# Optimization experiments

Hardware: AMD Instinct MI355X
Metric: run time of the kernel (lower is better)

Reference implementation:

```python
import jax, jax.numpy as jnp
import numpy as np

EMBED_DIM = 1024
NUM_HEADS = 16
HEAD_DIM = EMBED_DIM // NUM_HEADS


def setup_inputs() -> dict:
    key = jax.random.key(0)
    ks = jax.random.split(key, 11)
    B, S, D = 2, 2048, EMBED_DIM
    s = 1.0 / np.sqrt(D)
    inp = {
        "query": jax.random.normal(ks[0], (B, S, D), jnp.float32),
        "key": jax.random.normal(ks[1], (B, S, D), jnp.float32),
        "value": jax.random.normal(ks[2], (B, S, D), jnp.float32),
        # torch Linear weights: [out, in]
        "Wq": jax.random.normal(ks[3], (D, D), jnp.float32) * s,
        "bq": jnp.zeros((D,), jnp.float32),
        "Wk": jax.random.normal(ks[4], (D, D), jnp.float32) * s,
        "bk": jnp.zeros((D,), jnp.float32),
        "Wv": jax.random.normal(ks[5], (D, D), jnp.float32) * s,
        "bv": jnp.zeros((D,), jnp.float32),
        "Wo": jax.random.normal(ks[6], (D, D), jnp.float32) * s,
        "bo": jnp.zeros((D,), jnp.float32),
    }
    return inp


def reference(query, key, value, Wq, bq, Wk, bk, Wv, bv, Wo, bo):
    B, Q, D = query.shape
    K = key.shape[1]
    H, Hd = NUM_HEADS, HEAD_DIM
    # NOTE: source divides by scaling = head_dim**-0.5, i.e. multiplies by sqrt(head_dim)
    scaling = float(Hd) ** (-0.5)

    q = (query @ Wq.T + bq).reshape(B, Q, H, Hd).transpose(0, 2, 1, 3)  # [B,H,Q,Hd]
    k = (key @ Wk.T + bk).reshape(B, K, H, Hd).transpose(0, 2, 1, 3)    # [B,H,K,Hd]
    v = (value @ Wv.T + bv).reshape(B, K, H, Hd).transpose(0, 2, 1, 3)  # [B,H,K,Hd]

    scores = jnp.einsum("bhqd,bhkd->bhqk", q, k) / scaling
    attn = jax.nn.softmax(scores, axis=-1)  # dropout=0 (eval)
    out = jnp.einsum("bhqk,bhkd->bhqd", attn, v)
    out = out.transpose(0, 2, 1, 3).reshape(B, Q, D)
    return out @ Wo.T + bo
```

## Files before the change

### kernel.cpp

```cpp
#include <hip/hip_runtime.h>
#include <type_traits>
#include <utility>

#define B_ 2
#define S_ 2048
#define D_ 1024
#define H_ 16
#define HD_ 64
#define KDIM 1024

typedef __attribute__((ext_vector_type(8))) short    s16x8;
typedef __attribute__((ext_vector_type(8))) _Float16 h16x8;
typedef __attribute__((ext_vector_type(4))) float    f32x4;
typedef __attribute__((ext_vector_type(4))) int      i32x4;
typedef __attribute__((ext_vector_type(2))) int      i32x2;

template <typename T, typename = void> struct mfma_takes : std::false_type {};
template <typename T>
struct mfma_takes<T, std::void_t<decltype(__builtin_amdgcn_mfma_f32_16x16x32_f16(
    std::declval<T>(), std::declval<T>(), std::declval<f32x4>(), 0, 0, 0))>>
    : std::true_type {};
using frag8 = std::conditional_t<mfma_takes<h16x8>::value, h16x8, s16x8>;

__device__ __forceinline__ f32x4 mfma_f16(frag8 a, frag8 b, f32x4 c) {
  return __builtin_amdgcn_mfma_f32_16x16x32_f16(a, b, c, 0, 0, 0);
}

__device__ __forceinline__ short f2h(float f) {
  _Float16 h = (_Float16)f;
  short s; __builtin_memcpy(&s, &h, 2);
  return s;
}
__device__ __forceinline__ int pk2h(float a, float b) {
  auto p = __builtin_amdgcn_cvt_pkrtz(a, b);
  int r; __builtin_memcpy(&r, &p, 4); return r;
}
__device__ __forceinline__ frag8 ld_frag(const short* p) {
  return __builtin_bit_cast(frag8, *(const i32x4*)p);
}
__device__ __forceinline__ float fast_exp2(float x) {
  return __builtin_amdgcn_exp2f(x);
}

typedef __attribute__((address_space(1))) const void gvoid;
typedef __attribute__((address_space(3))) void lvoid;
__device__ __forceinline__ void async_copy16(const void* g, void* l) {
  __builtin_amdgcn_global_load_lds((gvoid*)g, (lvoid*)l, 16, 0, 0);
}

#define RAW_BARRIER() asm volatile("s_barrier" ::: "memory")
#define WAITCNT_VM(n) asm volatile("s_waitcnt vmcnt(" #n ")" ::: "memory")

__global__ __launch_bounds__(256)
void conv_all(const float* __restrict__ q, const float* __restrict__ k,
              const float* __restrict__ v, const float* __restrict__ Wq,
              const float* __restrict__ Wk, const float* __restrict__ Wv,
              const float* __restrict__ Wo,
              short* __restrict__ qh, short* __restrict__ kh,
              short* __restrict__ vh, short* __restrict__ wq,
              short* __restrict__ wk, short* __restrict__ wv,
              short* __restrict__ wo) {
  const int blk = blockIdx.x;
  const float* src; short* dst; int base;
  if (blk < 2048)      { src = q;  dst = qh; base = blk; }
  else if (blk < 4096) { src = k;  dst = kh; base = blk - 2048; }
  else if (blk < 6144) { src = v;  dst = vh; base = blk - 4096; }
  else if (blk < 6656) { src = Wq; dst = wq; base = blk - 6144; }
  else if (blk < 7168) { src = Wk; dst = wk; base = blk - 6656; }
  else if (blk < 7680) { src = Wv; dst = wv; base = blk - 7168; }
  else                 { src = Wo; dst = wo; base = blk - 7680; }
  const int i = base * 2048 + threadIdx.x * 8;
  float4 a0 = *(const float4*)(src + i);
  float4 a1 = *(const float4*)(src + i + 4);
  short h[8] = { f2h(a0.x), f2h(a0.y), f2h(a0.z), f2h(a0.w),
                 f2h(a1.x), f2h(a1.y), f2h(a1.z), f2h(a1.w) };
  i32x4 ph; __builtin_memcpy(&ph, h, 16);
  *(i32x4*)(dst + i) = ph;
}

__global__ __launch_bounds__(256, 3)
void gemm_qkv(const short* __restrict__ qh, const short* __restrict__ kh,
              const short* __restrict__ vh, const short* __restrict__ wq,
              const short* __restrict__ wk, const short* __restrict__ wv,
              const float* __restrict__ bq, const float* __restrict__ bk,
              const float* __restrict__ bv, short* __restrict__ Qf,
              short* __restrict__ Kf, short* __restrict__ Vt, float QS) {
  __shared__ short As[3 * 4096];
  __shared__ short Bs[3 * 4096];

  const int blk = blockIdx.x;
  const int xcd = blk & 7, i = blk >> 3;
  const int p = (i >> 3) * 8 + xcd;
  const int bn = i & 7;
  const int z = p >> 5, bm = p & 31;
  const short* Ap = z == 0 ? qh : z == 1 ? kh : vh;
  const short* Wp = z == 0 ? wq : z == 1 ? wk : wv;
  const float* bias = z == 0 ? bq : z == 1 ? bk : bv;
  short* Out = z == 0 ? Qf : z == 1 ? Kf : Vt;
  const float scale = z == 0 ? QS : 1.0f;
  const int omode = z == 2 ? 2 : 1;

  const int t = threadIdx.x, wave = t >> 6, lane = t & 63;
  const int laneN = lane & 15, quad = lane >> 4;
  const int wm = wave & 1, wn = wave >> 1;

  f32x4 acc[4][4];
#pragma unroll
  for (int i2 = 0; i2 < 4; ++i2)
#pragma unroll
    for (int j = 0; j < 4; ++j)
#pragma unroll
      for (int r = 0; r < 4; ++r) acc[i2][j][r] = 0.f;

  auto stage = [&](int buf, int kk) {
#pragma unroll
    for (int j = 0; j < 2; ++j) {
      const int chunk = j * 256 + t;
      const int row = chunk >> 2;
      const int gg = (chunk & 3) ^ ((row >> 1) & 3);
      async_copy16(Ap + (size_t)(bm * 128 + row) * KDIM + kk + gg * 8,
                   As + buf * 4096 + chunk * 8);
      async_copy16(Wp + (size_t)(bn * 128 + row) * KDIM + kk + gg * 8,
                   Bs + buf * 4096 + chunk * 8);
    }
  };

  stage(0, 0);
  stage(1, 32);
  int buf = 0;
  for (int kk = 0; kk < KDIM; kk += 32) {
    if (kk + 64 < KDIM) {
      int nb = buf + 2; if (nb >= 3) nb -= 3;
      stage(nb, kk + 64);
      WAITCNT_VM(8);
    } else if (kk + 32 < KDIM) {
      WAITCNT_VM(4);
    } else {
      WAITCNT_VM(0);
    }
    RAW_BARRIER();

    frag8 aF[4], bF[4];
#pragma unroll
    for (int mi = 0; mi < 4; ++mi) {
      const int row = wm * 64 + mi * 16 + laneN;
      aF[mi] = ld_frag(As + buf * 4096 + row * 32 +
                       ((quad ^ ((row >> 1) & 3)) * 8));
    }
#pragma unroll
    for (int ni = 0; ni < 4; ++ni) {
      const int row = wn * 64 + ni * 16 + laneN;
      bF[ni] = ld_frag(Bs + buf * 4096 + row * 32 +
                       ((quad ^ ((row >> 1) & 3)) * 8));
    }
#pragma unroll
    for (int mi = 0; mi < 4; ++mi)
#pragma unroll
      for (int ni = 0; ni < 4; ++ni)
        acc[mi][ni] = mfma_f16(aF[mi], bF[ni], acc[mi][ni]);
    RAW_BARRIER();
    buf = buf + 1 == 3 ? 0 : buf + 1;
  }

  short* scr = As + wave * 1152;
  const int h = bn * 2 + wn;
  if (omode == 2) {
    const int bidx = bm >> 4;
    const int sbase = (bm * 128 + wm * 64) & 2047;
#pragma unroll
    for (int ni = 0; ni < 4; ++ni) {
      const float bb = bias[bn * 128 + wn * 64 + ni * 16 + laneN];
#pragma unroll
      for (int mi = 0; mi < 4; ++mi) {
        short pk[4];
#pragma unroll
        for (int r = 0; r < 4; ++r) pk[r] = f2h(acc[mi][ni][r] + bb);
        i32x2 w; __builtin_memcpy(&w, pk, 8);
        *(i32x2*)(scr + laneN * 72 + mi * 16 + quad * 4) = w;
      }
#pragma unroll
      for (int j = 0; j < 2; ++j) {
        const int ff = lane * 2 + j, hdr = ff >> 3, ch = ff & 7;
        i32x4 v = *(const i32x4*)(scr + hdr * 72 + ch * 8);
        *(i32x4*)(Vt + (((size_t)(bidx * H_ + h)) * HD_ + ni * 16 + hdr) * S_ +
                  sbase + ch * 8) = v;
      }
    }
  } else {
#pragma unroll
    for (int mi = 0; mi < 4; ++mi) {
#pragma unroll
      for (int ni = 0; ni < 4; ++ni) {
        const float bb = bias[bn * 128 + wn * 64 + ni * 16 + laneN];
#pragma unroll
        for (int r = 0; r < 4; ++r)
          scr[(quad * 4 + r) * 72 + ni * 16 + laneN] =
              f2h((acc[mi][ni][r] + bb) * scale);
      }
#pragma unroll
      for (int j = 0; j < 2; ++j) {
        const int ff = lane * 2 + j, row = ff >> 3, ch = ff & 7;
        const int rowg = bm * 128 + wm * 64 + mi * 16 + row;
        const int bidx = rowg >> 11, s = rowg & 2047;
        i32x4 v = *(const i32x4*)(scr + row * 72 + ch * 8);
        *(i32x4*)(Out + (((size_t)(bidx * H_ + h)) * S_ + s) * HD_ + ch * 8) = v;
      }
    }
  }
}

__global__ __launch_bounds__(256, 3)
void gemm_out(const short* __restrict__ Ap, const short* __restrict__ Wp,
              const float* __restrict__ bias, float* __restrict__ Out) {
  __shared__ short As[3 * 4096];
  __shared__ short Bs[3 * 2048];
  const int blk = blockIdx.x;
  const int xcd = blk & 7, i = blk >> 3;
  const int bm = (i >> 4) * 8 + xcd;
  const int bn = i & 15;

  const int t = threadIdx.x, wave = t >> 6, lane = t & 63;
  const int laneN = lane & 15, quad = lane >> 4;
  const int wm = wave & 1, wn = wave >> 1;

  f32x4 acc[4][2];
#pragma unroll
  for (int i2 = 0; i2 < 4; ++i2)
#pragma unroll
    for (int j = 0; j < 2; ++j)
#pragma unroll
      for (int r = 0; r < 4; ++r) acc[i2][j][r] = 0.f;

  auto stage = [&](int buf, int kk) {
#pragma unroll
    for (int j = 0; j < 2; ++j) {
      const int chunk = j * 256 + t;
      const int row = chunk >> 2;
      const int gg = (chunk & 3) ^ ((row >> 1) & 3);
      async_copy16(Ap + (size_t)(bm * 128 + row) * KDIM + kk + gg * 8,
                   As + buf * 4096 + chunk * 8);
    }
    {
      const int chunk = t;
      const int row = chunk >> 2;
      const int gg = (chunk & 3) ^ ((row >> 1) & 3);
      async_copy16(Wp + (size_t)(bn * 64 + row) * KDIM + kk + gg * 8,
                   Bs + buf * 2048 + chunk * 8);
    }
  };

  stage(0, 0);
  stage(1, 32);
  int buf = 0;
  for (int kk = 0; kk < KDIM; kk += 32) {
    if (kk + 64 < KDIM) {
      int nb = buf + 2; if (nb >= 3) nb -= 3;
      stage(nb, kk + 64);
      WAITCNT_VM(6);
    } else if (kk + 32 < KDIM) {
      WAITCNT_VM(3);
    } else {
      WAITCNT_VM(0);
    }
    RAW_BARRIER();

    frag8 aF[4], bF[2];
#pragma unroll
    for (int mi = 0; mi < 4; ++mi) {
      const int row = wm * 64 + mi * 16 + laneN;
      aF[mi] = ld_frag(As + buf * 4096 + row * 32 +
                       ((quad ^ ((row >> 1) & 3)) * 8));
    }
#pragma unroll
    for (int ni = 0; ni < 2; ++ni) {
      const int row = wn * 32 + ni * 16 + laneN;
      bF[ni] = ld_frag(Bs + buf * 2048 + row * 32 +
                       ((quad ^ ((row >> 1) & 3)) * 8));
    }
#pragma unroll
    for (int mi = 0; mi < 4; ++mi)
#pragma unroll
      for (int ni = 0; ni < 2; ++ni)
        acc[mi][ni] = mfma_f16(aF[mi], bF[ni], acc[mi][ni]);
    RAW_BARRIER();
    buf = buf + 1 == 3 ? 0 : buf + 1;
  }

  float* scr = (float*)As + wave * 576;
#pragma unroll
  for (int mi = 0; mi < 4; ++mi) {
#pragma unroll
    for (int ni = 0; ni < 2; ++ni) {
      const float bb = bias[bn * 64 + wn * 32 + ni * 16 + laneN];
#pragma unroll
      for (int r = 0; r < 4; ++r)
        scr[(quad * 4 + r) * 36 + ni * 16 + laneN] = acc[mi][ni][r] + bb;
    }
#pragma unroll
    for (int j = 0; j < 2; ++j) {
      const int ff = lane * 2 + j, row = ff >> 3, ch = ff & 7;
      const int rowg = bm * 128 + wm * 64 + mi * 16 + row;
      f32x4 v = *(const f32x4*)(scr + row * 36 + ch * 4);
      *(f32x4*)(Out + (size_t)rowg * 1024 + bn * 64 + wn * 32 + ch * 4) = v;
    }
  }
}

__global__ __launch_bounds__(512, 4)
void attn(const short* __restrict__ Qf, const short* __restrict__ Kf,
          const short* __restrict__ Vt_, short* __restrict__ Ow) {
  __shared__ short Ks[4 * 4096];
  __shared__ short Vts[4 * 4096];
  __shared__ short Ps[8][16 * 64];

  const int blk = blockIdx.x;
  const int xcd = blk & 7, local = blk >> 3;
  const int pair = xcd * 4 + (local >> 4);
  const int h = pair & 15, b = pair >> 4, qt = local & 15;
  const size_t head = ((size_t)b * H_ + h) * (size_t)S_ * HD_;

  const int t = threadIdx.x;
  const int wave = t >> 6, lane = t & 63;
  const int laneN = lane & 15, quad = lane >> 4;

  frag8 qf[2];
  {
    const size_t row = (size_t)qt * 128 + wave * 16 + laneN;
#pragma unroll
    for (int half = 0; half < 2; ++half)
      qf[half] = ld_frag(Qf + head + row * HD_ + half * 32 + quad * 8);
  }

  f32x4 o[4];
  float m_r = -1e30f, l_r = 0.f;
#pragma unroll
  for (int i = 0; i < 4; ++i)
#pragma unroll
    for (int j = 0; j < 4; ++j) o[i][j] = 0.f;

  const int srow = t >> 3, sg = (t & 7) ^ (srow & 7);
  const short* kp = Kf + head + (size_t)srow * HD_ + sg * 8;
  const short* vp = Vt_ + head + (size_t)srow * S_ + sg * 8;
  const int d = t * 8;

  int off[4][2];
#pragma unroll
  for (int nt = 0; nt < 4; ++nt) {
    const int row = nt * 16 + laneN;
    off[nt][0] = row * 64 + ((quad ^ (row & 7)) * 8);
    off[nt][1] = row * 64 + (((quad + 4) ^ (row & 7)) * 8);
  }

  short* const pwr = &Ps[wave][0] + laneN * 64;
  short* pw[4];
#pragma unroll
  for (int nt = 0; nt < 4; ++nt) {
    const int g = nt * 2 + (quad >> 1);
    pw[nt] = pwr + ((g + laneN) & 7) * 8 + (quad & 1) * 4;
  }
  const short* prd0 = pwr + ((quad + laneN) & 7) * 8;
  const short* prd1 = pwr + (((quad + 4) + laneN) & 7) * 8;

  async_copy16(kp, Ks + d);  async_copy16(vp, Vts + d);
  kp += 4096; vp += 64;
  async_copy16(kp, Ks + 4096 + d);  async_copy16(vp, Vts + 4096 + d);
  kp += 4096; vp += 64;

#define ATTN_TILE(B0, STG)                                                   \
  {                                                                          \
    if (STG == 1) {                                                          \
      async_copy16(kp, Ks + (((B0) + 2) & 3) * 4096 + d);                    \
      async_copy16(vp, Vts + (((B0) + 2) & 3) * 4096 + d);                   \
      kp += 4096; vp += 64;                                                  \
      WAITCNT_VM(4);                                                         \
    } else if (STG == 2) {                                                   \
      WAITCNT_VM(2);                                                         \
    } else {                                                                 \
      WAITCNT_VM(0);                                                         \
    }                                                                        \
    RAW_BARRIER();                                                           \
    const short* KbS = Ks + (B0) * 4096;                                     \
    const short* VbS = Vts + (B0) * 4096;                                    \
                        \
    frag8 vf[4][2];                                                          \
    _Pragma("unroll")                                                        \
    for (int dt = 0; dt < 4; ++dt) {                                         \
      vf[dt][0] = ld_frag(VbS + off[dt][0]);                                 \
      vf[dt][1] = ld_frag(VbS + off[dt][1]);                                 \
    }                                                                        \
          \
    f32x4 s[4];                                                              \
    __builtin_amdgcn_s_setprio(1);                                           \
    _Pragma("unroll")                                                        \
    for (int nt = 0; nt < 4; ++nt) {                                         \
      frag8 k0 = ld_frag(KbS + off[nt][0]);                                  \
      frag8 k1 = ld_frag(KbS + off[nt][1]);                                  \
      f32x4 acc = {0.f, 0.f, 0.f, 0.f};                                      \
      acc = mfma_f16(k0, qf[0], acc);                                        \
      acc = mfma_f16(k1, qf[1], acc);                                        \
      s[nt] = acc;                                                           \
    }                                                                        \
    __builtin_amdgcn_s_setprio(0);                                           \
          \
    {                                                                        \
      float mt[4];                                                           \
      _Pragma("unroll")                                                      \
      for (int nt = 0; nt < 4; ++nt)                                         \
        mt[nt] = fmaxf(fmaxf(s[nt][0], s[nt][1]),                            \
                       fmaxf(s[nt][2], s[nt][3]));                           \
      float mx = fmaxf(fmaxf(mt[0], mt[1]), fmaxf(mt[2], mt[3]));            \
      mx = fmaxf(mx, __shfl_xor(mx, 16));                                    \
      mx = fmaxf(mx, __shfl_xor(mx, 32));                                    \
      if (__any(mx > m_r + 8.f)) {         \
        const float mn = fmaxf(m_r, mx);                                     \
        const float al = fast_exp2(m_r - mn);                                \
        m_r = mn;                                                            \
        l_r *= al;                                                           \
        _Pragma("unroll")                                                    \
        for (int dt = 0; dt < 4; ++dt)                                       \
          _Pragma("unroll")                                                  \
          for (int r = 0; r < 4; ++r) o[dt][r] *= al;                        \
      }                                                                      \
      float rt[4];                                                           \
      _Pragma("unroll")                                                      \
      for (int nt = 0; nt < 4; ++nt) {                                       \
        const float p0 = fast_exp2(s[nt][0] - m_r);                          \
        const float p1 = fast_exp2(s[nt][1] - m_r);                          \
        const float p2 = fast_exp2(s[nt][2] - m_r);                          \
        const float p3 = fast_exp2(s[nt][3] - m_r);                          \
        s[nt][0] = p0; s[nt][1] = p1; s[nt][2] = p2; s[nt][3] = p3;          \
        rt[nt] = (p0 + p1) + (p2 + p3);                                      \
      }                                                                      \
      float rs = (rt[0] + rt[1]) + (rt[2] + rt[3]);                          \
      rs += __shfl_xor(rs, 16);                                              \
      rs += __shfl_xor(rs, 32);                                              \
      l_r += rs;                                                             \
    }                                                                        \
            \
    _Pragma("unroll")                                                        \
    for (int nt = 0; nt < 4; ++nt) {                                         \
      i32x2 w;                                                               \
      w[0] = pk2h(s[nt][0], s[nt][1]);                                       \
      w[1] = pk2h(s[nt][2], s[nt][3]);                                       \
      *(i32x2*)pw[nt] = w;                                                   \
    }                                                                        \
          \
    const frag8 p0 = ld_frag(prd0);                                          \
    const frag8 p1 = ld_frag(prd1);                                          \
    __builtin_amdgcn_s_setprio(1);                                           \
    _Pragma("unroll")                                                        \
    for (int dt = 0; dt < 4; ++dt) {                                         \
      o[dt] = mfma_f16(vf[dt][0], p0, o[dt]);                                \
      o[dt] = mfma_f16(vf[dt][1], p1, o[dt]);                                \
    }                                                                        \
    __builtin_amdgcn_s_setprio(0);                                           \
  }

  for (int it = 0; it < 7; ++it) {
    ATTN_TILE(0, 1)
    ATTN_TILE(1, 1)
    ATTN_TILE(2, 1)
    ATTN_TILE(3, 1)
  }
  ATTN_TILE(0, 1)
  ATTN_TILE(1, 1)
  ATTN_TILE(2, 2)
  ATTN_TILE(3, 0)
#undef ATTN_TILE

  {
    const float inv = 1.0f / l_r;
    const int sgq = qt * 128 + wave * 16 + laneN;
    short* dst = Ow + ((size_t)b * S_ + sgq) * D_ + h * HD_;
#pragma unroll
    for (int dt = 0; dt < 4; ++dt) {
      short pk[4] = { f2h(o[dt][0] * inv), f2h(o[dt][1] * inv),
                      f2h(o[dt][2] * inv), f2h(o[dt][3] * inv) };
      i32x2 w; __builtin_memcpy(&w, pk, 8);
      *(i32x2*)(dst + dt * 16 + quad * 4) = w;
    }
  }
}

extern "C" void kernel_launch(void* const* d_in, const int* in_sizes, int n_in,
                              void* d_out, int out_size, void* d_ws, size_t ws_size,
                              hipStream_t stream) {
  const float* q  = (const float*)d_in[0];
  const float* k  = (const float*)d_in[1];
  const float* v  = (const float*)d_in[2];
  const float* Wq = (const float*)d_in[3];
  const float* bq = (const float*)d_in[4];
  const float* Wk = (const float*)d_in[5];
  const float* bk = (const float*)d_in[6];
  const float* Wv = (const float*)d_in[7];
  const float* bv = (const float*)d_in[8];
  const float* Wo = (const float*)d_in[9];
  const float* bo = (const float*)d_in[10];

  const size_t NTOK = (size_t)B_ * S_ * D_;
  const size_t NW   = (size_t)D_ * D_;
  short* p = (short*)d_ws;
  short* qh = p; p += NTOK;  short* kh = p; p += NTOK;  short* vh = p; p += NTOK;
  short* wq = p; p += NW;    short* wk = p; p += NW;
  short* wv = p; p += NW;    short* wo = p; p += NW;
  short* Qf = p; p += NTOK;  short* Kf = p; p += NTOK;
  short* Vt = p; p += NTOK;  short* Ow = p; p += NTOK;

  dim3 blk(256);

  conv_all<<<8192, blk, 0, stream>>>(q, k, v, Wq, Wk, Wv, Wo,
                                     qh, kh, vh, wq, wk, wv, wo);

  const float QS = 11.541560327111707f;
  gemm_qkv<<<768, blk, 0, stream>>>(qh, kh, vh, wq, wk, wv, bq, bk, bv,
                                    Qf, Kf, Vt, QS);

  attn<<<512, dim3(512), 0, stream>>>(Qf, Kf, Vt, Ow);

  gemm_out<<<512, blk, 0, stream>>>(Ow, wo, bo, (float*)d_out);
}
```

Before: 224.2 us.

## Software-pipeline QK^T one tile ahead in attention; widen out-proj K step to 64

The attention loop now computes the QK^T scores for the next K tile while the current tile's softmax and PV MFMAs run, so score MFMAs overlap the exp/max work. The prefetch wait counts are tightened so the next tile's K is resident one step earlier. Separately, the output-projection GEMM moves from a triple-buffered 32-wide K step to a double-buffered 64-wide K step with a new 8-way XOR swizzle and precomputed LDS offsets, halving barriers per K. This raises register pressure from the extra score fragments and reduces the prefetch distance in the GEMM.

```diff
diff --git a/kernel.cpp b/kernel.cpp
--- a/kernel.cpp
+++ b/kernel.cpp
@@ -212,8 +212,8 @@
 __global__ __launch_bounds__(256, 3)
 void gemm_out(const short* __restrict__ Ap, const short* __restrict__ Wp,
               const float* __restrict__ bias, float* __restrict__ Out) {
-  __shared__ short As[3 * 4096];
-  __shared__ short Bs[3 * 2048];
+  __shared__ short As[2 * 8192];
+  __shared__ short Bs[2 * 4096];
   const int blk = blockIdx.x;
   const int xcd = blk & 7, i = blk >> 3;
   const int bm = (i >> 4) * 8 + xcd;
@@ -233,57 +233,68 @@
 
   auto stage = [&](int buf, int kk) {
 #pragma unroll
+    for (int j = 0; j < 4; ++j) {
+      const int c = j * 256 + t;
+      const int row = c >> 3, g = (c & 7) ^ (row & 7);
+      async_copy16(Ap + (size_t)(bm * 128 + row) * KDIM + kk + g * 8,
+                   As + buf * 8192 + c * 8);
+    }
+#pragma unroll
     for (int j = 0; j < 2; ++j) {
-      const int chunk = j * 256 + t;
-      const int row = chunk >> 2;
-      const int gg = (chunk & 3) ^ ((row >> 1) & 3);
-      async_copy16(Ap + (size_t)(bm * 128 + row) * KDIM + kk + gg * 8,
-                   As + buf * 4096 + chunk * 8);
-    }
-    {
-      const int chunk = t;
-      const int row = chunk >> 2;
-      const int gg = (chunk & 3) ^ ((row >> 1) & 3);
-      async_copy16(Wp + (size_t)(bn * 64 + row) * KDIM + kk + gg * 8,
-                   Bs + buf * 2048 + chunk * 8);
+      const int c = j * 256 + t;
+      const int row = c >> 3, g = (c & 7) ^ (row & 7);
+      async_copy16(Wp + (size_t)(bn * 64 + row) * KDIM + kk + g * 8,
+                   Bs + buf * 4096 + c * 8);
     }
   };
 
+  int offA[4][2], offB[2][2];
+#pragma unroll
+  for (int mi = 0; mi < 4; ++mi) {
+    const int row = wm * 64 + mi * 16 + laneN;
+#pragma unroll
+    for (int ks = 0; ks < 2; ++ks)
+      offA[mi][ks] = row * 64 + (((quad + 4 * ks) ^ (row & 7)) * 8);
+  }
+#pragma unroll
+  for (int ni = 0; ni < 2; ++ni) {
+    const int row = wn * 32 + ni * 16 + laneN;
+#pragma unroll
+    for (int ks = 0; ks < 2; ++ks)
+      offB[ni][ks] = row * 64 + (((quad + 4 * ks) ^ (row & 7)) * 8);
+  }
+
   stage(0, 0);
-  stage(1, 32);
   int buf = 0;
-  for (int kk = 0; kk < KDIM; kk += 32) {
+  for (int kk = 0; kk < KDIM; kk += 64) {
     if (kk + 64 < KDIM) {
-      int nb = buf + 2; if (nb >= 3) nb -= 3;
-      stage(nb, kk + 64);
+      stage(buf ^ 1, kk + 64);
       WAITCNT_VM(6);
-    } else if (kk + 32 < KDIM) {
-      WAITCNT_VM(3);
     } else {
       WAITCNT_VM(0);
     }
     RAW_BARRIER();
 
-    frag8 aF[4], bF[2];
+    frag8 aF[4][2], bF[2][2];
 #pragma unroll
     for (int mi = 0; mi < 4; ++mi) {
-      const int row = wm * 64 + mi * 16 + laneN;
-      aF[mi] = ld_frag(As + buf * 4096 + row * 32 +
-                       ((quad ^ ((row >> 1) & 3)) * 8));
+      aF[mi][0] = ld_frag(As + buf * 8192 + offA[mi][0]);
+      aF[mi][1] = ld_frag(As + buf * 8192 + offA[mi][1]);
     }
 #pragma unroll
     for (int ni = 0; ni < 2; ++ni) {
-      const int row = wn * 32 + ni * 16 + laneN;
-      bF[ni] = ld_frag(Bs + buf * 2048 + row * 32 +
-                       ((quad ^ ((row >> 1) & 3)) * 8));
+      bF[ni][0] = ld_frag(Bs + buf * 4096 + offB[ni][0]);
+      bF[ni][1] = ld_frag(Bs + buf * 4096 + offB[ni][1]);
     }
 #pragma unroll
     for (int mi = 0; mi < 4; ++mi)
 #pragma unroll
-      for (int ni = 0; ni < 2; ++ni)
-        acc[mi][ni] = mfma_f16(aF[mi], bF[ni], acc[mi][ni]);
+      for (int ni = 0; ni < 2; ++ni) {
+        acc[mi][ni] = mfma_f16(aF[mi][0], bF[ni][0], acc[mi][ni]);
+        acc[mi][ni] = mfma_f16(aF[mi][1], bF[ni][1], acc[mi][ni]);
+      }
     RAW_BARRIER();
-    buf = buf + 1 == 3 ? 0 : buf + 1;
+    buf ^= 1;
   }
 
   float* scr = (float*)As + wave * 576;
@@ -366,42 +377,59 @@
   async_copy16(kp, Ks + 4096 + d);  async_copy16(vp, Vts + 4096 + d);
   kp += 4096; vp += 64;
 
-#define ATTN_TILE(B0, STG)                                                   \
+  f32x4 s[4];
+  WAITCNT_VM(2);
+  RAW_BARRIER();
+  {
+    __builtin_amdgcn_s_setprio(1);
+#pragma unroll
+    for (int nt = 0; nt < 4; ++nt) {
+      frag8 k0 = ld_frag(Ks + off[nt][0]);
+      frag8 k1 = ld_frag(Ks + off[nt][1]);
+      f32x4 acc = {0.f, 0.f, 0.f, 0.f};
+      acc = mfma_f16(k0, qf[0], acc);
+      acc = mfma_f16(k1, qf[1], acc);
+      s[nt] = acc;
+    }
+    __builtin_amdgcn_s_setprio(0);
+  }
+
+#define ATTN_TILE(B0, STG, QKN)                                              \
   {                                                                          \
     if (STG == 1) {                                                          \
       async_copy16(kp, Ks + (((B0) + 2) & 3) * 4096 + d);                    \
       async_copy16(vp, Vts + (((B0) + 2) & 3) * 4096 + d);                   \
       kp += 4096; vp += 64;                                                  \
-      WAITCNT_VM(4);                                                         \
+      WAITCNT_VM(2);                                                         \
     } else if (STG == 2) {                                                   \
-      WAITCNT_VM(2);                                                         \
-    } else {                                                                 \
       WAITCNT_VM(0);                                                         \
     }                                                                        \
     RAW_BARRIER();                                                           \
-    const short* KbS = Ks + (B0) * 4096;                                     \
     const short* VbS = Vts + (B0) * 4096;                                    \
-                        \
+                              \
     frag8 vf[4][2];                                                          \
     _Pragma("unroll")                                                        \
     for (int dt = 0; dt < 4; ++dt) {                                         \
       vf[dt][0] = ld_frag(VbS + off[dt][0]);                                 \
       vf[dt][1] = ld_frag(VbS + off[dt][1]);                                 \
     }                                                                        \
-          \
-    f32x4 s[4];                                                              \
-    __builtin_amdgcn_s_setprio(1);                                           \
-    _Pragma("unroll")                                                        \
-    for (int nt = 0; nt < 4; ++nt) {                                         \
-      frag8 k0 = ld_frag(KbS + off[nt][0]);                                  \
-      frag8 k1 = ld_frag(KbS + off[nt][1]);                                  \
-      f32x4 acc = {0.f, 0.f, 0.f, 0.f};                                      \
-      acc = mfma_f16(k0, qf[0], acc);                                        \
-      acc = mfma_f16(k1, qf[1], acc);                                        \
-      s[nt] = acc;                                                           \
-    }                                                                        \
-    __builtin_amdgcn_s_setprio(0);                                           \
-          \
+                         \
+    f32x4 sn[4];                                                             \
+    if (QKN) {                                                               \
+      const short* KbS = Ks + (((B0) + 1) & 3) * 4096;                       \
+      __builtin_amdgcn_s_setprio(1);                                         \
+      _Pragma("unroll")                                                      \
+      for (int nt = 0; nt < 4; ++nt) {                                       \
+        frag8 k0 = ld_frag(KbS + off[nt][0]);                                \
+        frag8 k1 = ld_frag(KbS + off[nt][1]);                                \
+        f32x4 acc = {0.f, 0.f, 0.f, 0.f};                                    \
+        acc = mfma_f16(k0, qf[0], acc);                                      \
+        acc = mfma_f16(k1, qf[1], acc);                                      \
+        sn[nt] = acc;                                                        \
+      }                                                                      \
+      __builtin_amdgcn_s_setprio(0);                                         \
+    }                                                                        \
+             \
     {                                                                        \
       float mt[4];                                                           \
       _Pragma("unroll")                                                      \
@@ -454,18 +482,22 @@
       o[dt] = mfma_f16(vf[dt][1], p1, o[dt]);                                \
     }                                                                        \
     __builtin_amdgcn_s_setprio(0);                                           \
+    if (QKN) {                                                               \
+      _Pragma("unroll")                                                      \
+      for (int nt = 0; nt < 4; ++nt) s[nt] = sn[nt];                         \
+    }                                                                        \
   }
 
   for (int it = 0; it < 7; ++it) {
-    ATTN_TILE(0, 1)
-    ATTN_TILE(1, 1)
-    ATTN_TILE(2, 1)
-    ATTN_TILE(3, 1)
-  }
-  ATTN_TILE(0, 1)
-  ATTN_TILE(1, 1)
-  ATTN_TILE(2, 2)
-  ATTN_TILE(3, 0)
+    ATTN_TILE(0, 1, 1)
+    ATTN_TILE(1, 1, 1)
+    ATTN_TILE(2, 1, 1)
+    ATTN_TILE(3, 1, 1)
+  }
+  ATTN_TILE(0, 1, 1)
+  ATTN_TILE(1, 1, 1)
+  ATTN_TILE(2, 2, 1)
+  ATTN_TILE(3, 0, 0)
 #undef ATTN_TILE
 
   {
```

Result: no change. 225.1 us (+0.4%).
